# Performance work log

Hardware: AMD Instinct MI355X
Metric: run time of the kernel (lower is better)

Reference implementation:

```python
import jax, jax.numpy as jnp
import numpy as np

N_NODES = 100000
N_EDGES = 1600000
D = 128          # gnn_input_size == gnn_hidden_size
N_LAYERS = 7
N_GRAPHS = 64
N_CLASSES = 10
SNN_IN, SNN_H = 512, 1024
SNN_BETA = 0.85


def setup_inputs() -> dict:
    key = jax.random.key(0)
    ks = jax.random.split(key, 16)
    s = 0.05  # keep activations tame through 7 relu layers
    return {
        "snn_x": jax.random.normal(ks[0], (N_GRAPHS, SNN_IN), jnp.float32),
        "x": jax.random.normal(ks[1], (N_NODES, D), jnp.float32),
        "edge_index": jax.random.randint(ks[2], (2, N_EDGES), 0, N_NODES, jnp.int64),
        "batch": jnp.sort(jax.random.randint(ks[3], (N_NODES,), 0, N_GRAPHS, jnp.int64)),
        "snn_w1": jax.random.normal(ks[4], (SNN_IN, SNN_H), jnp.float32) * s,
        "snn_b1": jax.random.normal(ks[5], (SNN_H,), jnp.float32) * s,
        "snn_w2": jax.random.normal(ks[6], (SNN_H, N_CLASSES), jnp.float32) * s,
        "snn_b2": jax.random.normal(ks[7], (N_CLASSES,), jnp.float32) * s,
        "conv_wrel": jax.random.normal(ks[8], (N_LAYERS, D, D), jnp.float32) * s,
        "conv_wroot": jax.random.normal(ks[9], (N_LAYERS, D, D), jnp.float32) * s,
        "conv_brel": jax.random.normal(ks[10], (N_LAYERS, D), jnp.float32) * s,
        "lin_w": jax.random.normal(ks[11], (D, N_CLASSES), jnp.float32) * s,
        "lin_b": jax.random.normal(ks[12], (N_CLASSES,), jnp.float32) * s,
        "fuse_w": jax.random.normal(ks[13], (2 * N_CLASSES, N_CLASSES), jnp.float32) * s,
        "fuse_b": jax.random.normal(ks[14], (N_CLASSES,), jnp.float32) * s,
    }


def reference(snn_x, x, edge_index, batch,
              snn_w1, snn_b1, snn_w2, snn_b2,
              conv_wrel, conv_wroot, conv_brel,
              lin_w, lin_b, fuse_w, fuse_b):
    n = x.shape[0]
    src, dst = edge_index[0], edge_index[1]
    h = x
    for i in range(conv_wrel.shape[0]):
        agg = jax.ops.segment_sum(h[src], dst, num_segments=n)  # gather + scatter-add
        h = jax.nn.relu(agg @ conv_wrel[i] + conv_brel[i] + h @ conv_wroot[i])
    # global_mean_pool over batch segments
    sums = jax.ops.segment_sum(h, batch, num_segments=N_GRAPHS)
    cnts = jax.ops.segment_sum(jnp.ones((n,), h.dtype), batch, num_segments=N_GRAPHS)
    pooled = sums / jnp.maximum(cnts, 1.0)[:, None]
    gnn_logits = pooled @ lin_w + lin_b
    # SNN branch
    snn_h = jax.nn.relu(snn_x @ snn_w1 + snn_b1)
    snn_logits = SNN_BETA * (snn_h @ snn_w2 + snn_b2)
    # fusion
    fused = jnp.concatenate([snn_logits, gnn_logits], axis=-1)
    return fused @ fuse_w + fuse_b
```

## Files before the change

kernel.cpp:

```cpp
#include <hip/hip_runtime.h>
#include <hip/hip_bf16.h>

#define N_NODES 100000
#define N_EDGES 1600000
#define DIM     128
#define N_LAYERS 7
#define N_GRAPHS 64
#define SNN_IN  512
#define SNN_HID 1024
#define NCLS    10
#define M_PAD   100096
#define MBLK    782
#define NBK     782
#define SORT_CHUNK 4096
#define SORT_NCH   391
#define XPAIRS  (N_NODES * 64)
#define WELEMS  (N_LAYERS * DIM * 256)

typedef __attribute__((ext_vector_type(8))) short short8;
typedef __attribute__((ext_vector_type(4))) float f32x4;

__device__ __forceinline__ unsigned int f2bf(float f) {
    unsigned int u = __float_as_uint(f);
    return (u + 0x7fffu + ((u >> 16) & 1u)) >> 16;
}
__device__ __forceinline__ float bf2f(unsigned short b) {
    return __uint_as_float(((unsigned int)b) << 16);
}
__device__ __forceinline__ void acc_pair(unsigned int u, float& lo, float& hi) {
    lo += __uint_as_float(u << 16);
    hi += __uint_as_float(u & 0xffff0000u);
}

__global__ void k_convert(const float* __restrict__ x, const float* __restrict__ wrel,
                          const float* __restrict__ wroot, unsigned int* __restrict__ h,
                          unsigned short* __restrict__ Wt) {
    int i = blockIdx.x * blockDim.x + threadIdx.x;
    if (i < XPAIRS) {
        float2 v = ((const float2*)x)[i];
        h[i] = f2bf(v.x) | (f2bf(v.y) << 16);
    } else {
        int idx = i - XPAIRS;
        if (idx < WELEMS) {
            int l = idx >> 15, rem = idx & 32767, n = rem >> 8, k = rem & 255;
            float v = (k < 128) ? wrel[l * 16384 + k * 128 + n]
                                : wroot[l * 16384 + (k - 128) * 128 + n];
            Wt[idx] = (unsigned short)f2bf(v);
        }
    }
}

__global__ __launch_bounds__(256) void k_histA(const int* __restrict__ dst,
                                               int* __restrict__ chunk_hist) {
    __shared__ int hist[NBK];
    int b = blockIdx.x, t = threadIdx.x;
    int e0 = b * SORT_CHUNK;
    int e1 = e0 + SORT_CHUNK; if (e1 > N_EDGES) e1 = N_EDGES;
    for (int i = t; i < NBK; i += 256) hist[i] = 0;
    __syncthreads();
    for (int e = e0 + t; e < e1; e += 256) atomicAdd(&hist[dst[e] >> 7], 1);
    __syncthreads();
    for (int i = t; i < NBK; i += 256) chunk_hist[b * NBK + i] = hist[i];
}

__global__ __launch_bounds__(64) void k_colscan(int* __restrict__ chunk_hist,
                                                int* __restrict__ btot) {
    int b = blockIdx.x;
    int lane = threadIdx.x;
    const int C = (SORT_NCH + 63) / 64;
    int vals[C]; int sum = 0;
    #pragma unroll
    for (int j = 0; j < C; j++) {
        int c = lane * C + j;
        vals[j] = (c < SORT_NCH) ? chunk_hist[c * NBK + b] : 0;
        sum += vals[j];
    }
    int s = sum;
    #pragma unroll
    for (int o = 1; o < 64; o <<= 1) { int t = __shfl_up(s, o); if (lane >= o) s += t; }
    if (lane == 63) btot[b] = s;
    int run = s - sum;
    #pragma unroll
    for (int j = 0; j < C; j++) {
        int c = lane * C + j;
        if (c < SORT_NCH) chunk_hist[c * NBK + b] = run;
        run += vals[j];
    }
}

__global__ __launch_bounds__(256) void k_bscan(const int* __restrict__ btot,
                                               int* __restrict__ bucket_base) {
    __shared__ int wsum[4];
    int tid = threadIdx.x, lane = tid & 63, wid = tid >> 6;
    int i0 = tid * 4;
    int v[4]; int sum = 0;
    #pragma unroll
    for (int j = 0; j < 4; j++) { int i = i0 + j; v[j] = (i < NBK) ? btot[i] : 0; sum += v[j]; }
    int s = sum;
    #pragma unroll
    for (int o = 1; o < 64; o <<= 1) { int t = __shfl_up(s, o); if (lane >= o) s += t; }
    if (lane == 63) wsum[wid] = s;
    __syncthreads();
    if (tid == 0) {
        int acc = 0;
        #pragma unroll
        for (int w = 0; w < 4; w++) { acc += wsum[w]; wsum[w] = acc; }
    }
    __syncthreads();
    int prefix = s - sum + (wid ? wsum[wid - 1] : 0);
    #pragma unroll
    for (int j = 0; j < 4; j++) { int i = i0 + j; if (i < NBK) bucket_base[i] = prefix; prefix += v[j]; }
}

__global__ __launch_bounds__(256) void k_scatterA(const int* __restrict__ src,
                                                  const int* __restrict__ dst,
                                                  const int* __restrict__ chunk_hist,
                                                  const int* __restrict__ bucket_base,
                                                  unsigned int* __restrict__ pairs) {
    __shared__ int lcur[NBK];
    int b = blockIdx.x, t = threadIdx.x;
    int e0 = b * SORT_CHUNK;
    int e1 = e0 + SORT_CHUNK; if (e1 > N_EDGES) e1 = N_EDGES;
    for (int i = t; i < NBK; i += 256) lcur[i] = chunk_hist[b * NBK + i] + bucket_base[i];
    __syncthreads();
    for (int e = e0 + t; e < e1; e += 256) {
        int d = dst[e];
        int bk = d >> 7;
        int pos = atomicAdd(&lcur[bk], 1);
        pairs[pos] = (unsigned int)src[e] | ((unsigned int)(d & 127) << 17);
    }
}

__global__ __launch_bounds__(256) void k_bucketB(const unsigned int* __restrict__ pairs,
                                                 const int* __restrict__ bucket_base,
                                                 const int* __restrict__ btot,
                                                 int* __restrict__ row_off,
                                                 int* __restrict__ sorted_src) {
    __shared__ int lcnt[128];
    __shared__ int loff[128];
    int b = blockIdx.x, t = threadIdx.x;
    int node0 = b << 7;
    int nn = N_NODES - node0; if (nn > 128) nn = 128;
    int base = bucket_base[b];
    int end  = base + btot[b];
    if (t < 128) lcnt[t] = 0;
    __syncthreads();
    for (int i = base + t; i < end; i += 256) atomicAdd(&lcnt[pairs[i] >> 17], 1);
    __syncthreads();
    if (t < 64) {
        int v0 = lcnt[2 * t], v1 = lcnt[2 * t + 1];
        int s = v0 + v1, ps = s;
        #pragma unroll
        for (int o = 1; o < 64; o <<= 1) { int u = __shfl_up(ps, o); if (t >= o) ps += u; }
        int excl = ps - s;
        loff[2 * t] = excl; loff[2 * t + 1] = excl + v0;
    }
    __syncthreads();
    if (t < nn) row_off[node0 + t] = base + loff[t];
    if (b == NBK - 1 && t == 0) row_off[N_NODES] = end;
    if (t < 128) lcnt[t] = 0;
    __syncthreads();
    for (int i = base + t; i < end; i += 256) {
        unsigned int p = pairs[i];
        int l = p >> 17;
        int pos = atomicAdd(&lcnt[l], 1);
        sorted_src[base + loff[l] + pos] = (int)(p & 0x1FFFFu);
    }
}

__global__ __launch_bounds__(256) void k_agg(const uint4* __restrict__ h4,
                                             const int* __restrict__ row_off,
                                             const int* __restrict__ sorted_src,
                                             uint4* __restrict__ agg4) {
    int wid = threadIdx.x >> 6;
    int lane = threadIdx.x & 63;
    int node = blockIdx.x * 4 + wid;
    if (node >= N_NODES) return;
    int sub = lane >> 4, li = lane & 15;
    int beg = row_off[node], end = row_off[node + 1];
    float a[8] = {0.f, 0.f, 0.f, 0.f, 0.f, 0.f, 0.f, 0.f};
    for (int base = beg; base < end; base += 32) {
        int sidx[8]; bool val[8];
        #pragma unroll
        for (int u = 0; u < 8; u++) {
            int e = base + 4 * u + sub;
            val[u] = e < end;
            sidx[u] = val[u] ? sorted_src[e] : 0;
        }
        uint4 r[8];
        #pragma unroll
        for (int u = 0; u < 8; u++) {
            if (val[u]) r[u] = h4[(size_t)sidx[u] * 16 + li];
            else        r[u] = make_uint4(0u, 0u, 0u, 0u);
        }
        #pragma unroll
        for (int u = 0; u < 8; u++) {
            acc_pair(r[u].x, a[0], a[1]); acc_pair(r[u].y, a[2], a[3]);
            acc_pair(r[u].z, a[4], a[5]); acc_pair(r[u].w, a[6], a[7]);
        }
    }
    #pragma unroll
    for (int i = 0; i < 8; i++) {
        a[i] += __shfl_xor(a[i], 16);
        a[i] += __shfl_xor(a[i], 32);
    }
    if (sub == 0) {
        uint4 o;
        o.x = f2bf(a[0]) | (f2bf(a[1]) << 16);
        o.y = f2bf(a[2]) | (f2bf(a[3]) << 16);
        o.z = f2bf(a[4]) | (f2bf(a[5]) << 16);
        o.w = f2bf(a[6]) | (f2bf(a[7]) << 16);
        agg4[(size_t)node * 16 + li] = o;
    }
}

__global__ __launch_bounds__(256) void k_gemm(const unsigned short* __restrict__ Ag,
                                              const unsigned short* __restrict__ H,
                                              const unsigned short* __restrict__ Wt,
                                              const float* __restrict__ bias,
                                              unsigned short* __restrict__ Hout) {
    __shared__ unsigned short Es[64 * 144];
    int tid = threadIdx.x;
    int lane = tid & 63, wid = tid >> 6;
    int wr = (wid >> 1) * 64, wc = (wid & 1) * 64;
    int row0 = blockIdx.x * 128;
    f32x4 acc[4][4] = {};

    int ksub = (lane >> 4) * 8;
    const unsigned short* Aga = Ag + (size_t)(row0 + wr + (lane & 15)) * 128 + ksub;
    const unsigned short* Ha  = H  + (size_t)(row0 + wr + (lane & 15)) * 128 + ksub;
    const unsigned short* Bb  = Wt + (size_t)(wc + (lane & 15)) * 256 + ksub;

    auto load_frags = [&](short8* a, short8* b, int s) {
        const unsigned short* ab = (s < 4 ? Aga : Ha) + (s & 3) * 32;
        #pragma unroll
        for (int mi = 0; mi < 4; mi++) a[mi] = *(const short8*)(ab + mi * 16 * 128);
        const unsigned short* bp = Bb + s * 32;
        #pragma unroll
        for (int ni = 0; ni < 4; ni++) b[ni] = *(const short8*)(bp + ni * 16 * 256);
    };
    auto do_mfma = [&](short8* a, short8* b) {
        #pragma unroll
        for (int mi = 0; mi < 4; mi++)
            #pragma unroll
            for (int ni = 0; ni < 4; ni++)
                acc[mi][ni] = __builtin_amdgcn_mfma_f32_16x16x32_bf16(a[mi], b[ni], acc[mi][ni], 0, 0, 0);
    };

    short8 a0[4], b0[4], a1[4], b1[4];
    load_frags(a0, b0, 0);
    #pragma unroll
    for (int s = 0; s < 8; s += 2) {
        load_frags(a1, b1, s + 1);
        do_mfma(a0, b0);
        if (s + 2 < 8) load_frags(a0, b0, s + 2);
        do_mfma(a1, b1);
    }

    int cb = wc + (lane & 15);
    int rs = (lane >> 4) * 4;
    #pragma unroll
    for (int p = 0; p < 2; ++p) {
        __syncthreads();
        if (wr == 64 * p) {
            #pragma unroll
            for (int ni = 0; ni < 4; ni++) {
                int col = cb + ni * 16;
                float bn = bias[col];
                #pragma unroll
                for (int mi = 0; mi < 4; mi++) {
                    int rloc = mi * 16 + rs;
                    #pragma unroll
                    for (int rr = 0; rr < 4; rr++) {
                        float v = acc[mi][ni][rr] + bn;
                        v = v > 0.f ? v : 0.f;
                        Es[(rloc + rr) * 144 + col] = (unsigned short)f2bf(v);
                    }
                }
            }
        }
        __syncthreads();
        int rloc = tid >> 2;
        int c4 = (tid & 3) * 4;
        uint4* gd = (uint4*)(Hout + (size_t)(row0 + 64 * p + rloc) * 128);
        const uint4* es = (const uint4*)(Es + (size_t)rloc * 144);
        #pragma unroll
        for (int j = 0; j < 4; j++) gd[c4 + j] = es[c4 + j];
    }
}

__global__ __launch_bounds__(128) void k_pool(const unsigned short* __restrict__ h,
                                              const int* __restrict__ batch,
                                              float* __restrict__ pooled, int* __restrict__ counts) {
    __shared__ int bsh[128];
    int start = blockIdx.x * 128, t = threadIdx.x;
    int end = start + 128; if (end > N_NODES) end = N_NODES;
    int nn = end - start;
    if (t < nn) bsh[t] = batch[start + t];
    __syncthreads();
    float acc = 0.f; int cur = -1, cnt = 0;
    for (int i = 0; i < nn; i++) {
        int g = bsh[i];
        if (g != cur) {
            if (cur >= 0) { atomicAdd(&pooled[cur * 128 + t], acc); if (t == 0) atomicAdd(&counts[cur], cnt); }
            cur = g; acc = 0.f; cnt = 0;
        }
        acc += bf2f(h[(size_t)(start + i) * 128 + t]);
        cnt++;
    }
    if (cur >= 0) { atomicAdd(&pooled[cur * 128 + t], acc); if (t == 0) atomicAdd(&counts[cur], cnt); }
}

__global__ __launch_bounds__(256) void k_snn1(const float* __restrict__ x, const float* __restrict__ w1,
                                              const float* __restrict__ b1, float* __restrict__ out) {
    __shared__ float xs[SNN_IN];
    int m = blockIdx.x, tid = threadIdx.x;
    for (int i = tid; i < SNN_IN; i += 256) xs[i] = x[m * SNN_IN + i];
    __syncthreads();
    float a0 = 0.f, a1 = 0.f, a2 = 0.f, a3 = 0.f;
    for (int k = 0; k < SNN_IN; k++) {
        float xv = xs[k];
        const float* wr = w1 + (size_t)k * SNN_HID + tid;
        a0 += xv * wr[0]; a1 += xv * wr[256]; a2 += xv * wr[512]; a3 += xv * wr[768];
    }
    float v;
    v = a0 + b1[tid];       out[m * SNN_HID + tid]       = v > 0.f ? v : 0.f;
    v = a1 + b1[tid + 256]; out[m * SNN_HID + tid + 256] = v > 0.f ? v : 0.f;
    v = a2 + b1[tid + 512]; out[m * SNN_HID + tid + 512] = v > 0.f ? v : 0.f;
    v = a3 + b1[tid + 768]; out[m * SNN_HID + tid + 768] = v > 0.f ? v : 0.f;
}

__global__ __launch_bounds__(64) void k_head(const float* __restrict__ pooled, const int* __restrict__ counts,
                                             const float* __restrict__ lin_w, const float* __restrict__ lin_b,
                                             const float* __restrict__ snn_h, const float* __restrict__ w2,
                                             const float* __restrict__ b2, const float* __restrict__ fuse_w,
                                             const float* __restrict__ fuse_b, float* __restrict__ out) {
    int m = blockIdx.x, lane = threadIdx.x;
    __shared__ float sm[20];
    float cnt = (float)(counts[m] > 0 ? counts[m] : 1);
    float p0 = pooled[m * 128 + lane] / cnt;
    float p1 = pooled[m * 128 + 64 + lane] / cnt;
    for (int c = 0; c < NCLS; c++) {
        float v = p0 * lin_w[lane * 10 + c] + p1 * lin_w[(lane + 64) * 10 + c];
        #pragma unroll
        for (int o = 32; o > 0; o >>= 1) v += __shfl_down(v, o);
        if (lane == 0) sm[10 + c] = v + lin_b[c];
    }
    for (int c = 0; c < NCLS; c++) {
        float v = 0.f;
        #pragma unroll
        for (int j = 0; j < 16; j++) {
            int k = lane + j * 64;
            v += snn_h[m * SNN_HID + k] * w2[k * 10 + c];
        }
        #pragma unroll
        for (int o = 32; o > 0; o >>= 1) v += __shfl_down(v, o);
        if (lane == 0) sm[c] = 0.85f * (v + b2[c]);
    }
    __syncthreads();
    if (lane < NCLS) {
        float o = fuse_b[lane];
        #pragma unroll
        for (int j = 0; j < 20; j++) o += sm[j] * fuse_w[j * 10 + lane];
        out[m * 10 + lane] = o;
    }
}

extern "C" void kernel_launch(void* const* d_in, const int* in_sizes, int n_in,
                              void* d_out, int out_size, void* d_ws, size_t ws_size,
                              hipStream_t stream) {
    const float* snn_x  = (const float*)d_in[0];
    const float* x      = (const float*)d_in[1];
    const int*   ei     = (const int*)d_in[2];
    const int*   batch  = (const int*)d_in[3];
    const float* w1     = (const float*)d_in[4];
    const float* b1     = (const float*)d_in[5];
    const float* w2     = (const float*)d_in[6];
    const float* b2     = (const float*)d_in[7];
    const float* wrel   = (const float*)d_in[8];
    const float* wroot  = (const float*)d_in[9];
    const float* brel   = (const float*)d_in[10];
    const float* lin_w  = (const float*)d_in[11];
    const float* lin_b  = (const float*)d_in[12];
    const float* fuse_w = (const float*)d_in[13];
    const float* fuse_b = (const float*)d_in[14];
    const int* srcv = ei;
    const int* dstv = ei + N_EDGES;

    char* ws = (char*)d_ws;
    size_t off = 0;
    auto alloc = [&](size_t b) { char* p = ws + off; off = (off + b + 255) & ~(size_t)255; return p; };
    unsigned short* h0   = (unsigned short*)alloc((size_t)M_PAD * 128 * 2);
    unsigned short* h1   = (unsigned short*)alloc((size_t)M_PAD * 128 * 2);
    unsigned short* agg  = (unsigned short*)alloc((size_t)M_PAD * 128 * 2);
    unsigned short* Wt   = (unsigned short*)alloc((size_t)N_LAYERS * 128 * 256 * 2);
    int* sorted_src = (int*)alloc((size_t)N_EDGES * 4);
    unsigned int* pairs = (unsigned int*)alloc((size_t)N_EDGES * 4);
    int* chunk_hist = (int*)alloc((size_t)SORT_NCH * NBK * 4);
    int* row_off    = (int*)alloc((size_t)(N_NODES + 1) * 4);
    int* btot       = (int*)alloc((size_t)NBK * 4);
    int* bucket_base= (int*)alloc((size_t)NBK * 4);
    float* pooled   = (float*)alloc((size_t)N_GRAPHS * 128 * 4);
    int* counts     = (int*)alloc((size_t)N_GRAPHS * 4);
    float* snn_h    = (float*)alloc((size_t)N_GRAPHS * SNN_HID * 4);

    hipMemsetAsync(pooled, 0, (size_t)N_GRAPHS * 128 * 4, stream);
    hipMemsetAsync(counts, 0, (size_t)N_GRAPHS * 4, stream);

    k_histA<<<SORT_NCH, 256, 0, stream>>>(dstv, chunk_hist);
    k_colscan<<<NBK, 64, 0, stream>>>(chunk_hist, btot);
    k_bscan<<<1, 256, 0, stream>>>(btot, bucket_base);
    k_scatterA<<<SORT_NCH, 256, 0, stream>>>(srcv, dstv, chunk_hist, bucket_base, pairs);
    k_bucketB<<<NBK, 256, 0, stream>>>(pairs, bucket_base, btot, row_off, sorted_src);
    k_convert<<<(XPAIRS + WELEMS + 255) / 256, 256, 0, stream>>>(x, wrel, wroot, (unsigned int*)h0, Wt);

    unsigned short* hc = h0;
    unsigned short* hn = h1;
    for (int l = 0; l < N_LAYERS; l++) {
        k_agg<<<(N_NODES + 3) / 4, 256, 0, stream>>>((const uint4*)hc, row_off, sorted_src, (uint4*)agg);
        k_gemm<<<MBLK, 256, 0, stream>>>(agg, hc, Wt + (size_t)l * 128 * 256, brel + l * 128, hn);
        unsigned short* t = hc; hc = hn; hn = t;
    }
    k_pool<<<(N_NODES + 127) / 128, 128, 0, stream>>>(hc, batch, pooled, counts);
    k_snn1<<<N_GRAPHS, 256, 0, stream>>>(snn_x, w1, b1, snn_h);
    k_head<<<N_GRAPHS, 64, 0, stream>>>(pooled, counts, lin_w, lin_b, snn_h, w2, b2, fuse_w, fuse_b,
                                        (float*)d_out);
}
```

Measured before the change: 1.014 ms.

## Fuse neighbor aggregation into GraphConv GEMM via shared-memory tile

Merges the per-layer aggregation and GEMM kernels into one kernel. Each 128-row block first gathers and sums neighbor features for its nodes into a padded LDS tile, then runs the MFMA GEMM reading the aggregated half from LDS and the root half from global memory. This removes the agg buffer's global write and re-read plus one launch per layer. The cost is lower gather parallelism: each wave now walks 32 nodes serially with 4-way unrolling instead of 8, the GEMM loses its double-buffered fragment loads, and the 34 KB of LDS limits occupancy.

```diff
diff --git a/kernel.cpp b/kernel.cpp
--- a/kernel.cpp
+++ b/kernel.cpp
@@ -168,95 +168,87 @@
     }
 }
 
-__global__ __launch_bounds__(256) void k_agg(const uint4* __restrict__ h4,
-                                             const int* __restrict__ row_off,
-                                             const int* __restrict__ sorted_src,
-                                             uint4* __restrict__ agg4) {
-    int wid = threadIdx.x >> 6;
-    int lane = threadIdx.x & 63;
-    int node = blockIdx.x * 4 + wid;
-    if (node >= N_NODES) return;
-    int sub = lane >> 4, li = lane & 15;
-    int beg = row_off[node], end = row_off[node + 1];
-    float a[8] = {0.f, 0.f, 0.f, 0.f, 0.f, 0.f, 0.f, 0.f};
-    for (int base = beg; base < end; base += 32) {
-        int sidx[8]; bool val[8];
-        #pragma unroll
-        for (int u = 0; u < 8; u++) {
-            int e = base + 4 * u + sub;
-            val[u] = e < end;
-            sidx[u] = val[u] ? sorted_src[e] : 0;
-        }
-        uint4 r[8];
-        #pragma unroll
-        for (int u = 0; u < 8; u++) {
-            if (val[u]) r[u] = h4[(size_t)sidx[u] * 16 + li];
-            else        r[u] = make_uint4(0u, 0u, 0u, 0u);
-        }
-        #pragma unroll
-        for (int u = 0; u < 8; u++) {
-            acc_pair(r[u].x, a[0], a[1]); acc_pair(r[u].y, a[2], a[3]);
-            acc_pair(r[u].z, a[4], a[5]); acc_pair(r[u].w, a[6], a[7]);
-        }
-    }
-    #pragma unroll
-    for (int i = 0; i < 8; i++) {
-        a[i] += __shfl_xor(a[i], 16);
-        a[i] += __shfl_xor(a[i], 32);
-    }
-    if (sub == 0) {
-        uint4 o;
-        o.x = f2bf(a[0]) | (f2bf(a[1]) << 16);
-        o.y = f2bf(a[2]) | (f2bf(a[3]) << 16);
-        o.z = f2bf(a[4]) | (f2bf(a[5]) << 16);
-        o.w = f2bf(a[6]) | (f2bf(a[7]) << 16);
-        agg4[(size_t)node * 16 + li] = o;
-    }
-}
-
-__global__ __launch_bounds__(256) void k_gemm(const unsigned short* __restrict__ Ag,
-                                              const unsigned short* __restrict__ H,
-                                              const unsigned short* __restrict__ Wt,
-                                              const float* __restrict__ bias,
-                                              unsigned short* __restrict__ Hout) {
-    __shared__ unsigned short Es[64 * 144];
+__global__ __launch_bounds__(256, 4) void k_fconv(const uint4* __restrict__ h4,
+                                                  const unsigned short* __restrict__ H,
+                                                  const unsigned short* __restrict__ Wt,
+                                                  const float* __restrict__ bias,
+                                                  const int* __restrict__ row_off,
+                                                  const int* __restrict__ sorted_src,
+                                                  unsigned short* __restrict__ Hout) {
+    __shared__ unsigned short As[128 * 136];
     int tid = threadIdx.x;
     int lane = tid & 63, wid = tid >> 6;
+    int row0 = blockIdx.x * 128;
+    int sub = lane >> 4, li = lane & 15;
+
+    #pragma unroll 1
+    for (int i = 0; i < 32; i++) {
+        int nl = (wid << 5) + i;
+        int node = row0 + nl;
+        float a[8] = {0.f, 0.f, 0.f, 0.f, 0.f, 0.f, 0.f, 0.f};
+        if (node < N_NODES) {
+            int beg = row_off[node], end = row_off[node + 1];
+            for (int base = beg; base < end; base += 16) {
+                int sidx[4]; bool val[4];
+                #pragma unroll
+                for (int u = 0; u < 4; u++) {
+                    int e = base + 4 * u + sub;
+                    val[u] = e < end;
+                    sidx[u] = val[u] ? sorted_src[e] : 0;
+                }
+                uint4 r[4];
+                #pragma unroll
+                for (int u = 0; u < 4; u++) {
+                    if (val[u]) r[u] = h4[(size_t)sidx[u] * 16 + li];
+                    else        r[u] = make_uint4(0u, 0u, 0u, 0u);
+                }
+                #pragma unroll
+                for (int u = 0; u < 4; u++) {
+                    acc_pair(r[u].x, a[0], a[1]); acc_pair(r[u].y, a[2], a[3]);
+                    acc_pair(r[u].z, a[4], a[5]); acc_pair(r[u].w, a[6], a[7]);
+                }
+            }
+            #pragma unroll
+            for (int j = 0; j < 8; j++) {
+                a[j] += __shfl_xor(a[j], 16);
+                a[j] += __shfl_xor(a[j], 32);
+            }
+        }
+        if (sub == 0) {
+            uint4 o;
+            o.x = f2bf(a[0]) | (f2bf(a[1]) << 16);
+            o.y = f2bf(a[2]) | (f2bf(a[3]) << 16);
+            o.z = f2bf(a[4]) | (f2bf(a[5]) << 16);
+            o.w = f2bf(a[6]) | (f2bf(a[7]) << 16);
+            *(uint4*)&As[nl * 136 + li * 8] = o;
+        }
+    }
+    __syncthreads();
+
     int wr = (wid >> 1) * 64, wc = (wid & 1) * 64;
-    int row0 = blockIdx.x * 128;
     f32x4 acc[4][4] = {};
-
     int ksub = (lane >> 4) * 8;
-    const unsigned short* Aga = Ag + (size_t)(row0 + wr + (lane & 15)) * 128 + ksub;
-    const unsigned short* Ha  = H  + (size_t)(row0 + wr + (lane & 15)) * 128 + ksub;
-    const unsigned short* Bb  = Wt + (size_t)(wc + (lane & 15)) * 256 + ksub;
-
-    auto load_frags = [&](short8* a, short8* b, int s) {
-        const unsigned short* ab = (s < 4 ? Aga : Ha) + (s & 3) * 32;
-        #pragma unroll
-        for (int mi = 0; mi < 4; mi++) a[mi] = *(const short8*)(ab + mi * 16 * 128);
-        const unsigned short* bp = Bb + s * 32;
-        #pragma unroll
-        for (int ni = 0; ni < 4; ni++) b[ni] = *(const short8*)(bp + ni * 16 * 256);
-    };
-    auto do_mfma = [&](short8* a, short8* b) {
+    const unsigned short* Al = As + (wr + (lane & 15)) * 136 + ksub;
+    const unsigned short* Ha = H + (size_t)(row0 + wr + (lane & 15)) * 128 + ksub;
+    const unsigned short* Bb = Wt + (size_t)(wc + (lane & 15)) * 256 + ksub;
+    #pragma unroll
+    for (int s = 0; s < 8; s++) {
+        short8 a[4], b[4];
+        #pragma unroll
+        for (int mi = 0; mi < 4; mi++) {
+            if (s < 4) a[mi] = *(const short8*)(Al + mi * 16 * 136 + s * 32);
+            else       a[mi] = *(const short8*)(Ha + mi * 16 * 128 + (s - 4) * 32);
+        }
+        #pragma unroll
+        for (int ni = 0; ni < 4; ni++) b[ni] = *(const short8*)(Bb + s * 32 + ni * 16 * 256);
         #pragma unroll
         for (int mi = 0; mi < 4; mi++)
             #pragma unroll
             for (int ni = 0; ni < 4; ni++)
                 acc[mi][ni] = __builtin_amdgcn_mfma_f32_16x16x32_bf16(a[mi], b[ni], acc[mi][ni], 0, 0, 0);
-    };
-
-    short8 a0[4], b0[4], a1[4], b1[4];
-    load_frags(a0, b0, 0);
-    #pragma unroll
-    for (int s = 0; s < 8; s += 2) {
-        load_frags(a1, b1, s + 1);
-        do_mfma(a0, b0);
-        if (s + 2 < 8) load_frags(a0, b0, s + 2);
-        do_mfma(a1, b1);
-    }
-
+    }
+
+    unsigned short* Es = As;
     int cb = wc + (lane & 15);
     int rs = (lane >> 4) * 4;
     #pragma unroll
@@ -392,7 +384,6 @@
     auto alloc = [&](size_t b) { char* p = ws + off; off = (off + b + 255) & ~(size_t)255; return p; };
     unsigned short* h0   = (unsigned short*)alloc((size_t)M_PAD * 128 * 2);
     unsigned short* h1   = (unsigned short*)alloc((size_t)M_PAD * 128 * 2);
-    unsigned short* agg  = (unsigned short*)alloc((size_t)M_PAD * 128 * 2);
     unsigned short* Wt   = (unsigned short*)alloc((size_t)N_LAYERS * 128 * 256 * 2);
     int* sorted_src = (int*)alloc((size_t)N_EDGES * 4);
     unsigned int* pairs = (unsigned int*)alloc((size_t)N_EDGES * 4);
@@ -417,8 +408,8 @@
     unsigned short* hc = h0;
     unsigned short* hn = h1;
     for (int l = 0; l < N_LAYERS; l++) {
-        k_agg<<<(N_NODES + 3) / 4, 256, 0, stream>>>((const uint4*)hc, row_off, sorted_src, (uint4*)agg);
-        k_gemm<<<MBLK, 256, 0, stream>>>(agg, hc, Wt + (size_t)l * 128 * 256, brel + l * 128, hn);
+        k_fconv<<<MBLK, 256, 0, stream>>>((const uint4*)hc, hc, Wt + (size_t)l * 128 * 256,
+                                          brel + l * 128, row_off, sorted_src, hn);
         unsigned short* t = hc; hc = hn; hn = t;
     }
     k_pool<<<(N_NODES + 127) / 128, 128, 0, stream>>>(hc, batch, pooled, counts);
```

Measured after the change: 1.098 ms. 1.08x slower.
